# Kernel optimization log

Measured on AMD Instinct MI355X. Metric: run time of the kernel, lower is better.

## Reference

```python
import jax, jax.numpy as jnp
import numpy as np

MAX_SHIFT_BANDS = 2.0


def setup_inputs() -> dict:
    key = jax.random.key(0)
    k1, k2 = jax.random.split(key)
    B, Bh, H, W = 4, 128, 256, 256
    x = jax.random.normal(k1, (B, Bh, H, W), dtype=jnp.float32)
    wavelength_shift = jax.random.normal(k2, (B, Bh, W), dtype=jnp.float32)
    return {"x": x, "wavelength_shift": wavelength_shift}


def reference(x, wavelength_shift):
    # Faithful to torch grid_sample(mode='bilinear', padding_mode='border',
    # align_corners=False) applied along the spectral (band) axis only.
    B, Bh, H, W = x.shape
    dt = x.dtype

    shift = jnp.clip(wavelength_shift, -MAX_SHIFT_BANDS, MAX_SHIFT_BANDS)
    shift = shift[:, :, None, :]                         # [B,Bh,1,W]
    band = jnp.arange(Bh, dtype=dt)[None, :, None, None]  # [1,Bh,1,1]
    shifted = jnp.clip(band + shift, 0.0, Bh - 1)        # [B,Bh,1,W]

    # grid_sample align_corners=False unnormalization:
    # grid g = shifted/(Bh-1)*2 - 1 ; iy = ((g+1)*Bh - 1)/2 = shifted*Bh/(Bh-1) - 0.5
    iy = shifted * (Bh / (Bh - 1)) - 0.5                 # [B,Bh,1,W]
    i0f = jnp.floor(iy)
    w = iy - i0f                                          # lerp weight, [B,Bh,1,W]
    i0 = i0f.astype(jnp.int32)                            # may be -1 at low edge
    i0c = jnp.clip(i0, 0, Bh - 1)                         # border padding
    i1c = jnp.clip(i0 + 1, 0, Bh - 1)

    # broadcast gather indices over H rows
    i0c = jnp.broadcast_to(i0c, (B, Bh, H, W))
    i1c = jnp.broadcast_to(i1c, (B, Bh, H, W))

    x0 = jnp.take_along_axis(x, i0c, axis=1)              # [B,Bh,H,W]
    x1 = jnp.take_along_axis(x, i1c, axis=1)
    return x0 * (1.0 - w) + x1 * w
```

## Files before the change

kernel.cpp:

```cpp
#include <hip/hip_runtime.h>


#define BH_ 128
#define H_  256
#define W_  256
#define BG   16
#define NR   22

__global__ __launch_bounds__(256, 7) void smile_kernel(
    const float* __restrict__ x,
    const float* __restrict__ ws,
    float* __restrict__ out)
{
    __shared__ float tile[4][NR * 64];

    const int t    = threadIdx.x;
    const int wv   = t >> 6;
    const int lane = t & 63;

    const int bid0 = blockIdx.x;
    const int bid  = (bid0 & 7) * 1024 + (bid0 >> 3);

    const int bgb = bid & 1;
    int rem = bid >> 1;
    const int wg  = rem & 3;
    rem >>= 2;
    const int h   = rem & (H_ - 1);
    const int b   = rem >> 8;

    const int bg  = bgb * 4 + wv;
    const int bh0 = bg * BG;
    const int w   = wg * 64 + lane;

    float* const tl = &tile[wv][0];

#pragma unroll
    for (int i = 0; i < NR; ++i) {
        const int band = min(max(bh0 - 3 + i, 0), BH_ - 1);
        const float* gp = x + ((size_t)(b * BH_ + band) * H_ + h) * W_ + w;
        __builtin_amdgcn_global_load_lds(
            (const __attribute__((address_space(1))) void*)gp,
            (__attribute__((address_space(3))) void*)&tl[i * 64],
            4, 0, 0);
    }

    const float* __restrict__ wsp = ws + (size_t)(b * BH_ + bh0) * W_ + w;
    float s[BG];
#pragma unroll
    for (int r = 0; r < BG; ++r)
        s[r] = wsp[r * W_];

    asm volatile("s_waitcnt vmcnt(0)" ::: "memory");

    const float scale = (float)(128.0 / 127.0);
    float* __restrict__ outp =
        out + ((size_t)(b * BH_ + bh0) * H_ + h) * W_ + w;

#pragma unroll
    for (int r = 0; r < BG; ++r) {
        const int bh  = bh0 + r;
        float sc      = fminf(fmaxf(s[r], -2.0f), 2.0f);
        float shifted = fminf(fmaxf((float)bh + sc, 0.0f), (float)(BH_ - 1));
        float iy      = fmaf(shifted, scale, -0.5f);
        float i0f     = floorf(iy);
        float frac    = iy - i0f;
        int   i0      = (int)i0f;
        int   r0      = min(max(i0, 0), BH_ - 1) - (bh0 - 3);
        int   r1      = min(i0 + 1, BH_ - 1) - (bh0 - 3);
        float x0 = tl[r0 * 64 + lane];
        float x1 = tl[r1 * 64 + lane];
        __builtin_nontemporal_store(fmaf(frac, x1 - x0, x0),
                                    outp + (size_t)r * (H_ * W_));
    }
}

extern "C" void kernel_launch(void* const* d_in, const int* in_sizes, int n_in,
                              void* d_out, int out_size, void* d_ws, size_t ws_size,
                              hipStream_t stream) {
    const float* x  = (const float*)d_in[0];
    const float* ws = (const float*)d_in[1];
    float* out = (float*)d_out;

    const int grid = 8192;
    smile_kernel<<<grid, 256, 0, stream>>>(x, ws, out);
}
```

Measured before the change: 45.44 us.

## Retile to 4-band by 16-row blocks with 16-byte LDS staging loop

Restructures the work split so each block owns 4 bands across a 16-row strip and the full width, instead of one row with 16 bands per wave. Each block loops over pairs of rows, staging 10 halo bands into LDS with 16-byte global-to-LDS loads separated by barriers. Shift indices are computed once and reused across all rows in the strip. In exchange, halo reads grow relative to useful output (10 bands loaded per 4 produced), and each step waits on its loads with no overlap between loading and computing.

```diff
diff --git a/kernel.cpp b/kernel.cpp
--- a/kernel.cpp
+++ b/kernel.cpp
@@ -4,73 +4,87 @@
 #define BH_ 128
 #define H_  256
 #define W_  256
-#define BG   16
-#define NR   22
+#define NB   10
+#define CH    2
+#define HC   16
+#define NSTEP (HC / CH)
 
-__global__ __launch_bounds__(256, 7) void smile_kernel(
+__global__ __launch_bounds__(256) void smile_kernel(
     const float* __restrict__ x,
     const float* __restrict__ ws,
     float* __restrict__ out)
 {
-    __shared__ float tile[4][NR * 64];
+    __shared__ float stg[NB][CH][W_];
 
     const int t    = threadIdx.x;
     const int wv   = t >> 6;
     const int lane = t & 63;
 
     const int bid0 = blockIdx.x;
-    const int bid  = (bid0 & 7) * 1024 + (bid0 >> 3);
+    const int bid  = (bid0 & 7) * 256 + (bid0 >> 3);
 
-    const int bgb = bid & 1;
-    int rem = bid >> 1;
-    const int wg  = rem & 3;
-    rem >>= 2;
-    const int h   = rem & (H_ - 1);
-    const int b   = rem >> 8;
+    const int hc = bid & 15;
+    int rem = bid >> 4;
+    const int bg = rem & 31;
+    const int b  = rem >> 5;
+    const int bh0 = bg * 4;
+    const int h0  = hc * HC;
 
-    const int bg  = bgb * 4 + wv;
-    const int bh0 = bg * BG;
-    const int w   = wg * 64 + lane;
-
-    float* const tl = &tile[wv][0];
-
-#pragma unroll
-    for (int i = 0; i < NR; ++i) {
-        const int band = min(max(bh0 - 3 + i, 0), BH_ - 1);
-        const float* gp = x + ((size_t)(b * BH_ + band) * H_ + h) * W_ + w;
-        __builtin_amdgcn_global_load_lds(
-            (const __attribute__((address_space(1))) void*)gp,
-            (__attribute__((address_space(3))) void*)&tl[i * 64],
-            4, 0, 0);
-    }
-
-    const float* __restrict__ wsp = ws + (size_t)(b * BH_ + bh0) * W_ + w;
-    float s[BG];
-#pragma unroll
-    for (int r = 0; r < BG; ++r)
-        s[r] = wsp[r * W_];
-
-    asm volatile("s_waitcnt vmcnt(0)" ::: "memory");
+    const int bh = bh0 + wv;
 
     const float scale = (float)(128.0 / 127.0);
-    float* __restrict__ outp =
-        out + ((size_t)(b * BH_ + bh0) * H_ + h) * W_ + w;
-
+    const float* __restrict__ wsp = ws + (size_t)(b * BH_ + bh) * W_ + lane;
+    int r0[4], r1[4];
+    float fr[4];
 #pragma unroll
-    for (int r = 0; r < BG; ++r) {
-        const int bh  = bh0 + r;
-        float sc      = fminf(fmaxf(s[r], -2.0f), 2.0f);
+    for (int j = 0; j < 4; ++j) {
+        float sc      = fminf(fmaxf(wsp[j * 64], -2.0f), 2.0f);
         float shifted = fminf(fmaxf((float)bh + sc, 0.0f), (float)(BH_ - 1));
         float iy      = fmaf(shifted, scale, -0.5f);
         float i0f     = floorf(iy);
-        float frac    = iy - i0f;
-        int   i0      = (int)i0f;
-        int   r0      = min(max(i0, 0), BH_ - 1) - (bh0 - 3);
-        int   r1      = min(i0 + 1, BH_ - 1) - (bh0 - 3);
-        float x0 = tl[r0 * 64 + lane];
-        float x1 = tl[r1 * 64 + lane];
-        __builtin_nontemporal_store(fmaf(frac, x1 - x0, x0),
-                                    outp + (size_t)r * (H_ * W_));
+        fr[j]         = iy - i0f;
+        int i0        = (int)i0f;
+        r0[j] = min(max(i0, 0), BH_ - 1) - (bh0 - 3);
+        r1[j] = min(i0 + 1, BH_ - 1) - (bh0 - 3);
+    }
+
+    const float* __restrict__ xb = x + (size_t)b * (BH_ * H_ * W_);
+    float* __restrict__ outp =
+        out + ((size_t)(b * BH_ + bh) * H_ + h0) * W_ + lane;
+
+    for (int st = 0; st < NSTEP; ++st) {
+        const int hh = h0 + st * CH;
+
+#pragma unroll
+        for (int k = 0; k < 5; ++k) {
+            const int u    = wv + 4 * k;
+            const int bl   = u >> 1;
+            const int ch   = u & 1;
+            const int band = min(max(bh0 - 3 + bl, 0), BH_ - 1);
+            const float* gp = xb + ((size_t)band * H_ + (hh + ch)) * W_ + lane * 4;
+            __builtin_amdgcn_global_load_lds(
+                (const __attribute__((address_space(1))) void*)gp,
+                (__attribute__((address_space(3))) void*)&stg[bl][ch][0],
+                16, 0, 0);
+        }
+
+        asm volatile("s_waitcnt vmcnt(0)" ::: "memory");
+        __builtin_amdgcn_s_barrier();
+
+#pragma unroll
+        for (int ch = 0; ch < CH; ++ch) {
+#pragma unroll
+            for (int j = 0; j < 4; ++j) {
+                const int w = lane + j * 64;
+                float x0 = stg[r0[j]][ch][w];
+                float x1 = stg[r1[j]][ch][w];
+                __builtin_nontemporal_store(
+                    fmaf(fr[j], x1 - x0, x0),
+                    outp + (size_t)(st * CH + ch) * W_ + j * 64);
+            }
+        }
+
+        __builtin_amdgcn_s_barrier();
     }
 }
 
@@ -81,6 +95,6 @@
     const float* ws = (const float*)d_in[1];
     float* out = (float*)d_out;
 
-    const int grid = 8192;
+    const int grid = 4 * 32 * 16;
     smile_kernel<<<grid, 256, 0, stream>>>(x, ws, out);
 }
```

Result: slower. 46.86 us (+3.1%).
